# Kernel optimization log

Measured on AMD Instinct MI355X. Metric: run time of the kernel, lower is better.

The kernel has to match this reference:

```python
import jax, jax.numpy as jnp
import numpy as np

HEADS = 16
DIM_HEAD = 64


def setup_inputs() -> dict:
    key = jax.random.key(0)
    k1, k2, k3, k4, k5 = jax.random.split(key, 5)
    B, S, E = 4, 2048, 1024
    inner = HEADS * DIM_HEAD  # 1024
    return {
        "hidden_states": jax.random.normal(k1, (B, S, E), dtype=jnp.float32),
        "w_q": jax.random.normal(k2, (E, inner), dtype=jnp.float32) * (E ** -0.5),
        "w_k": jax.random.normal(k3, (E, inner), dtype=jnp.float32) * (E ** -0.5),
        "w_v": jax.random.normal(k4, (E, inner), dtype=jnp.float32) * (E ** -0.5),
        "w_o": jax.random.normal(k5, (inner, E), dtype=jnp.float32) * (inner ** -0.5),
    }


def reference(hidden_states, w_q, w_k, w_v, w_o):
    # Self-attention path: context = hidden_states (context arg is None).
    B, S, _ = hidden_states.shape
    dtype = hidden_states.dtype
    scale = DIM_HEAD ** -0.5

    q = (hidden_states @ w_q).reshape(B, S, HEADS, DIM_HEAD)
    k = (hidden_states @ w_k).reshape(B, S, HEADS, DIM_HEAD)
    v = (hidden_states @ w_v).reshape(B, S, HEADS, DIM_HEAD)

    # fp32 softmax as in the original module
    q32 = q.astype(jnp.float32)
    k32 = k.astype(jnp.float32)
    scores = jnp.einsum('btnh,bfnh->bnft', k32, q32) * scale  # [B, H, S_q, S_kv]
    probs = jax.nn.softmax(scores, axis=-1).astype(dtype)

    out = jnp.einsum('bnft,btnh->bfnh', probs, v)  # [B, S, H, D]
    out = out.reshape(B, S, HEADS * DIM_HEAD)
    return out @ w_o  # [B, S, query_dim]
```

## Files before the change

kernel.cpp:

```cpp
#include <hip/hip_runtime.h>
#include <stdint.h>

typedef __attribute__((ext_vector_type(8))) unsigned short ushort8;
typedef __attribute__((ext_vector_type(8))) __bf16 bf16x8;
typedef __attribute__((ext_vector_type(4))) float f32x4;
typedef __attribute__((ext_vector_type(4))) uint32_t u32x4;

#define TBK 32

__device__ __forceinline__ unsigned short f2bf(float f) {
  union { float f; uint32_t u; } x; x.f = f;
  uint32_t u = x.u;
  uint32_t r = (u + 0x7fffu + ((u >> 16) & 1u)) >> 16;
  return (unsigned short)r;
}

__device__ __forceinline__ uint32_t pack_bf2(float lo, float hi) {
  return (uint32_t)f2bf(lo) | ((uint32_t)f2bf(hi) << 16);
}

__device__ __forceinline__ uint32_t rhu2(float lo, float hi) {
  union { float f; uint32_t u; } a, b; a.f = lo; b.f = hi;
  return __builtin_amdgcn_perm(b.u + 0x8000u, a.u + 0x8000u, 0x07060302u);
}

__device__ __forceinline__ void store_c(unsigned short* p, float v) { *p = f2bf(v); }
__device__ __forceinline__ void store_c(float* p, float v) { *p = v; }

__device__ __forceinline__ void gll16(const unsigned short* g, unsigned short* l) {
  __builtin_amdgcn_global_load_lds((const __attribute__((address_space(1))) void*)g,
                                   (__attribute__((address_space(3))) void*)l,
                                   16, 0, 0);
}

__global__ __launch_bounds__(256) void cvt_f32_bf16(
    const float* __restrict__ x, unsigned short* __restrict__ y, int n4) {
  int i = blockIdx.x * 256 + threadIdx.x;
  if (i >= n4) return;
  float4 v = *(const float4*)(x + (size_t)i * 4);
  uint2 p; p.x = pack_bf2(v.x, v.y); p.y = pack_bf2(v.z, v.w);
  *(uint2*)(y + (size_t)i * 4) = p;
}

__global__ void transpose_w(const float* __restrict__ W,
                            unsigned short* __restrict__ WT) {
  __shared__ unsigned short tile[32][33];
  int c0 = blockIdx.x * 32, r0 = blockIdx.y * 32;
  int x = threadIdx.x, y = threadIdx.y;
#pragma unroll
  for (int i = 0; i < 32; i += 8)
    tile[y + i][x] = f2bf(W[(size_t)(r0 + y + i) * 1024 + c0 + x]);
  __syncthreads();
#pragma unroll
  for (int i = 0; i < 32; i += 8)
    WT[(size_t)(c0 + y + i) * 1024 + r0 + x] = tile[x][y + i];
}

template <typename OutT>
__global__ __launch_bounds__(256) void gemm_bt(
    const unsigned short* A,
    const unsigned short* BT0, const unsigned short* BT1, const unsigned short* BT2,
    OutT* C0, OutT* C1, OutT* C2,
    int M, int N, int K, float sc0) {
  const unsigned short* BT = (blockIdx.z == 0) ? BT0 : (blockIdx.z == 1) ? BT1 : BT2;
  OutT* C = (blockIdx.z == 0) ? C0 : (blockIdx.z == 1) ? C1 : C2;
  const float sc = (blockIdx.z == 0) ? sc0 : 1.0f;

  __shared__ __attribute__((aligned(16))) unsigned short As[128 * TBK];
  __shared__ __attribute__((aligned(16))) unsigned short Bs[128 * TBK];

  const int tid = threadIdx.x;
  const int wave = tid >> 6, lane = tid & 63;
  const int fr = lane & 15, fq = lane >> 4;
  const int bm = blockIdx.x * 128, bn = blockIdx.y * 128;
  const int wm = (wave >> 1) * 64, wn = (wave & 1) * 64;

  f32x4 acc[4][4] = {};

  const int sr = lane >> 2;
  const int sk = (lane & 3) * 8;
  const unsigned short* Ag = A + (size_t)(bm + wave * 32 + sr) * K + sk;
  const unsigned short* Bg = BT + (size_t)(bn + wave * 32 + sr) * K + sk;
  unsigned short* As0 = &As[(wave * 32) * TBK];
  unsigned short* Bs0 = &Bs[(wave * 32) * TBK];

  for (int k0 = 0; k0 < K; k0 += TBK) {
    gll16(Ag + k0, As0);
    gll16(Ag + k0 + 16 * K, As0 + 16 * TBK);
    gll16(Bg + k0, Bs0);
    gll16(Bg + k0 + 16 * K, Bs0 + 16 * TBK);
    asm volatile("s_waitcnt vmcnt(0)" ::: "memory");
    __syncthreads();

    bf16x8 af[4], bfr[4];
#pragma unroll
    for (int mt = 0; mt < 4; mt++)
      af[mt] = *(const bf16x8*)&As[(wm + mt * 16 + fr) * TBK + fq * 8];
#pragma unroll
    for (int nt = 0; nt < 4; nt++)
      bfr[nt] = *(const bf16x8*)&Bs[(wn + nt * 16 + fr) * TBK + fq * 8];
#pragma unroll
    for (int mt = 0; mt < 4; mt++)
#pragma unroll
      for (int nt = 0; nt < 4; nt++)
        acc[mt][nt] = __builtin_amdgcn_mfma_f32_16x16x32_bf16(af[mt], bfr[nt], acc[mt][nt], 0, 0, 0);
    __syncthreads();
  }

#pragma unroll
  for (int mt = 0; mt < 4; mt++)
#pragma unroll
    for (int nt = 0; nt < 4; nt++)
#pragma unroll
      for (int r = 0; r < 4; r++) {
        int row = bm + wm + mt * 16 + fq * 4 + r;
        int col = bn + wn + nt * 16 + fr;
        store_c(&C[(size_t)row * N + col], acc[mt][nt][r] * sc);
      }
}

__global__ __launch_bounds__(256, 4) void attn_kernel(
    const unsigned short* q, const unsigned short* k,
    const unsigned short* v, unsigned short* o) {
  const int S = 2048, E = 1024;
  __shared__ __attribute__((aligned(16))) unsigned short Ksb[2 * 64 * 64];
  __shared__ __attribute__((aligned(16))) unsigned short Vtb[2 * 64 * 64];

  const int tid = threadIdx.x;
  const int wave = tid >> 6, lane = tid & 63;
  const int fr = lane & 15, fq = lane >> 4;
  const int q0 = blockIdx.x * 128;
  const int bh = blockIdx.y;
  const int b = bh >> 4, h = bh & 15;
  const size_t base = ((size_t)b * S) * E + (size_t)h * 64;

  bf16x8 aq[2][2];
#pragma unroll
  for (int qg = 0; qg < 2; qg++)
#pragma unroll
    for (int ks = 0; ks < 2; ks++)
      aq[qg][ks] = *(const bf16x8*)&q[base +
          (size_t)(q0 + qg * 64 + wave * 16 + fr) * E + ks * 32 + fq * 8];

  ushort8 ones_u;
#pragma unroll
  for (int j = 0; j < 8; j++) ones_u[j] = 0x3F80;
  bf16x8 onesf = *(bf16x8*)&ones_u;

  f32x4 ot[2][4] = {};
  f32x4 osum[2] = {};

  const int srow = lane >> 3;
  const int scol = (((lane & 7) ^ srow) << 3);
  const unsigned short* Kg = k + base + (size_t)(wave * 16 + srow) * E + scol;
  unsigned short* KsW0 = &Ksb[wave * 1024];

  const int rp = (tid & 31) * 2;
  const int dcv = (tid >> 5) * 8;
  const int u_ = rp & 31;
  const int slot = 32 * (rp >> 5) + 8 * ((u_ & 15) >> 2) + 4 * (u_ >> 4) + (u_ & 3);
  const unsigned short* Vg = v + base + (size_t)rp * E + dcv;

  const int rx = (fr & 7) << 3;

  {
    gll16(Kg, KsW0);
    gll16(Kg + 8 * (size_t)E, KsW0 + 512);
    u32x4 a = *(const u32x4*)(Vg);
    u32x4 bb = *(const u32x4*)(Vg + E);
#pragma unroll
    for (int w = 0; w < 4; w++) {
      uint32_t lo = __builtin_amdgcn_perm(bb[w], a[w], 0x05040100u);
      uint32_t hi = __builtin_amdgcn_perm(bb[w], a[w], 0x07060302u);
      int d = dcv + 2 * w;
      *(uint32_t*)&Vtb[d * 64 + (slot ^ ((2 * w) << 3))] = lo;
      *(uint32_t*)&Vtb[(d + 1) * 64 + (slot ^ ((2 * w + 1) << 3))] = hi;
    }
    asm volatile("s_waitcnt vmcnt(0)" ::: "memory");
  }
  __syncthreads();

  int cur = 0;
  for (int t = 0; t < 32; t++) {
    const int nxt = cur ^ 4096;
    const bool pf = (t < 31);
    u32x4 va, vb;
    if (pf) {
      const size_t toff = (size_t)((t + 1) * 64) * E;
      va = *(const u32x4*)(Vg + toff);
      vb = *(const u32x4*)(Vg + toff + E);
      gll16(Kg + toff, &Ksb[nxt + wave * 1024]);
      gll16(Kg + toff + 8 * (size_t)E, &Ksb[nxt + wave * 1024 + 512]);
    }

    f32x4 st[2][4] = {};
#pragma unroll
    for (int ks = 0; ks < 2; ks++) {
#pragma unroll
      for (int tt = 0; tt < 4; tt++) {
        bf16x8 ak = *(const bf16x8*)&Ksb[cur + (tt * 16 + fr) * 64 +
                                         ((ks * 32 + fq * 8) ^ rx)];
        st[0][tt] = __builtin_amdgcn_mfma_f32_16x16x32_bf16(ak, aq[0][ks], st[0][tt], 0, 0, 0);
        st[1][tt] = __builtin_amdgcn_mfma_f32_16x16x32_bf16(ak, aq[1][ks], st[1][tt], 0, 0, 0);
      }
    }

    uint32_t pk[2][4][2];
#pragma unroll
    for (int qg = 0; qg < 2; qg++)
#pragma unroll
      for (int tt = 0; tt < 4; tt++) {
        float e0 = __builtin_amdgcn_exp2f(st[qg][tt][0]);
        float e1 = __builtin_amdgcn_exp2f(st[qg][tt][1]);
        float e2 = __builtin_amdgcn_exp2f(st[qg][tt][2]);
        float e3 = __builtin_amdgcn_exp2f(st[qg][tt][3]);
        pk[qg][tt][0] = rhu2(e0, e1);
        pk[qg][tt][1] = rhu2(e2, e3);
      }

    if (pf) {
#pragma unroll
      for (int w = 0; w < 4; w++) {
        uint32_t lo = __builtin_amdgcn_perm(vb[w], va[w], 0x05040100u);
        uint32_t hi = __builtin_amdgcn_perm(vb[w], va[w], 0x07060302u);
        int d = dcv + 2 * w;
        *(uint32_t*)&Vtb[nxt + d * 64 + (slot ^ ((2 * w) << 3))] = lo;
        *(uint32_t*)&Vtb[nxt + (d + 1) * 64 + (slot ^ ((2 * w + 1) << 3))] = hi;
      }
    }

#pragma unroll
    for (int c = 0; c < 2; c++) {
      bf16x8 bp[2];
#pragma unroll
      for (int qg = 0; qg < 2; qg++) {
        u32x4 bpr;
        bpr[0] = pk[qg][2 * c][0];
        bpr[1] = pk[qg][2 * c][1];
        bpr[2] = pk[qg][2 * c + 1][0];
        bpr[3] = pk[qg][2 * c + 1][1];
        bp[qg] = *(bf16x8*)&bpr;
      }
#pragma unroll
      for (int dt = 0; dt < 4; dt++) {
        bf16x8 av = *(const bf16x8*)&Vtb[cur + (dt * 16 + fr) * 64 +
                                         ((c * 32 + fq * 8) ^ rx)];
        ot[0][dt] = __builtin_amdgcn_mfma_f32_16x16x32_bf16(av, bp[0], ot[0][dt], 0, 0, 0);
        ot[1][dt] = __builtin_amdgcn_mfma_f32_16x16x32_bf16(av, bp[1], ot[1][dt], 0, 0, 0);
      }
      osum[0] = __builtin_amdgcn_mfma_f32_16x16x32_bf16(onesf, bp[0], osum[0], 0, 0, 0);
      osum[1] = __builtin_amdgcn_mfma_f32_16x16x32_bf16(onesf, bp[1], osum[1], 0, 0, 0);
    }

    if (pf) asm volatile("s_waitcnt vmcnt(0)" ::: "memory");
    __syncthreads();
    cur = nxt;
  }

#pragma unroll
  for (int qg = 0; qg < 2; qg++) {
    float inv = 1.0f / osum[qg][0];
    size_t rowbase = base + (size_t)(q0 + qg * 64 + wave * 16 + fr) * E;
#pragma unroll
    for (int dt = 0; dt < 4; dt++) {
      uint32_t w0 = rhu2(ot[qg][dt][0] * inv, ot[qg][dt][1] * inv);
      uint32_t w1 = rhu2(ot[qg][dt][2] * inv, ot[qg][dt][3] * inv);
      *(uint32_t*)&o[rowbase + dt * 16 + fq * 4] = w0;
      *(uint32_t*)&o[rowbase + dt * 16 + fq * 4 + 2] = w1;
    }
  }
}

extern "C" void kernel_launch(void* const* d_in, const int* in_sizes, int n_in,
                              void* d_out, int out_size, void* d_ws, size_t ws_size,
                              hipStream_t stream) {
  const float* hs = (const float*)d_in[0];
  const float* wq = (const float*)d_in[1];
  const float* wk = (const float*)d_in[2];
  const float* wv = (const float*)d_in[3];
  const float* wo = (const float*)d_in[4];
  unsigned short* ws = (unsigned short*)d_ws;

  unsigned short* wqT = ws;
  unsigned short* wkT = ws + 1048576;
  unsigned short* wvT = ws + 2097152;
  unsigned short* woT = wqT;
  unsigned short* qb  = ws + 3145728;
  unsigned short* kb  = qb + 8388608;
  unsigned short* vb  = kb + 8388608;
  unsigned short* ob  = qb;
  unsigned short* hsb = (unsigned short*)d_out;
  float* out = (float*)d_out;

  const int M = 8192, N = 1024, K = 1024;
  const float KSC = 0.125f * 1.44269504088896341f;

  cvt_f32_bf16<<<dim3(M * K / 4 / 256), 256, 0, stream>>>(hs, hsb, M * K / 4);

  dim3 tb(32, 8);
  transpose_w<<<dim3(32, 32), tb, 0, stream>>>(wq, wqT);
  transpose_w<<<dim3(32, 32), tb, 0, stream>>>(wk, wkT);
  transpose_w<<<dim3(32, 32), tb, 0, stream>>>(wv, wvT);

  gemm_bt<unsigned short><<<dim3(M / 128, N / 128, 3), 256, 0, stream>>>(
      hsb, wqT, wkT, wvT, qb, kb, vb, M, N, K, KSC);

  transpose_w<<<dim3(32, 32), tb, 0, stream>>>(wo, woT);

  attn_kernel<<<dim3(2048 / 128, 64), 256, 0, stream>>>(qb, kb, vb, ob);

  gemm_bt<float><<<dim3(M / 128, N / 128, 1), 256, 0, stream>>>(
      ob, woT, woT, woT, out, out, out, M, N, K, 1.0f);
}
```

Before: 296.8 us.

## Single-buffer V tile in attention loop and raise MFMA wave priority

```diff
diff --git a/kernel.cpp b/kernel.cpp
--- a/kernel.cpp
+++ b/kernel.cpp
@@ -124,7 +124,7 @@
     const unsigned short* v, unsigned short* o) {
   const int S = 2048, E = 1024;
   __shared__ __attribute__((aligned(16))) unsigned short Ksb[2 * 64 * 64];
-  __shared__ __attribute__((aligned(16))) unsigned short Vtb[2 * 64 * 64];
+  __shared__ __attribute__((aligned(16))) unsigned short Vtb[64 * 64];
 
   const int tid = threadIdx.x;
   const int wave = tid >> 6, lane = tid & 63;
@@ -153,7 +153,6 @@
   const int srow = lane >> 3;
   const int scol = (((lane & 7) ^ srow) << 3);
   const unsigned short* Kg = k + base + (size_t)(wave * 16 + srow) * E + scol;
-  unsigned short* KsW0 = &Ksb[wave * 1024];
 
   const int rp = (tid & 31) * 2;
   const int dcv = (tid >> 5) * 8;
@@ -163,37 +162,38 @@
 
   const int rx = (fr & 7) << 3;
 
-  {
-    gll16(Kg, KsW0);
-    gll16(Kg + 8 * (size_t)E, KsW0 + 512);
-    u32x4 a = *(const u32x4*)(Vg);
-    u32x4 bb = *(const u32x4*)(Vg + E);
+  gll16(Kg, &Ksb[wave * 1024]);
+  gll16(Kg + 8 * (size_t)E, &Ksb[wave * 1024 + 512]);
+
+  int cur = 0;
+  for (int t = 0; t < 32; t++) {
+    const int nxt = cur ^ 4096;
+
+    const size_t toff = (size_t)t * 64 * E;
+    u32x4 va = *(const u32x4*)(Vg + toff);
+    u32x4 vb = *(const u32x4*)(Vg + toff + E);
+
+    __syncthreads();
+
 #pragma unroll
     for (int w = 0; w < 4; w++) {
-      uint32_t lo = __builtin_amdgcn_perm(bb[w], a[w], 0x05040100u);
-      uint32_t hi = __builtin_amdgcn_perm(bb[w], a[w], 0x07060302u);
+      uint32_t lo = __builtin_amdgcn_perm(vb[w], va[w], 0x05040100u);
+      uint32_t hi = __builtin_amdgcn_perm(vb[w], va[w], 0x07060302u);
       int d = dcv + 2 * w;
       *(uint32_t*)&Vtb[d * 64 + (slot ^ ((2 * w) << 3))] = lo;
       *(uint32_t*)&Vtb[(d + 1) * 64 + (slot ^ ((2 * w + 1) << 3))] = hi;
     }
-    asm volatile("s_waitcnt vmcnt(0)" ::: "memory");
-  }
-  __syncthreads();
-
-  int cur = 0;
-  for (int t = 0; t < 32; t++) {
-    const int nxt = cur ^ 4096;
-    const bool pf = (t < 31);
-    u32x4 va, vb;
-    if (pf) {
-      const size_t toff = (size_t)((t + 1) * 64) * E;
-      va = *(const u32x4*)(Vg + toff);
-      vb = *(const u32x4*)(Vg + toff + E);
-      gll16(Kg + toff, &Ksb[nxt + wave * 1024]);
-      gll16(Kg + toff + 8 * (size_t)E, &Ksb[nxt + wave * 1024 + 512]);
+
+    __syncthreads();
+
+    if (t < 31) {
+      const size_t poff = (size_t)(t + 1) * 64 * E;
+      gll16(Kg + poff, &Ksb[nxt + wave * 1024]);
+      gll16(Kg + poff + 8 * (size_t)E, &Ksb[nxt + wave * 1024 + 512]);
     }
 
     f32x4 st[2][4] = {};
+    __builtin_amdgcn_s_setprio(1);
 #pragma unroll
     for (int ks = 0; ks < 2; ks++) {
 #pragma unroll
@@ -204,6 +204,7 @@
         st[1][tt] = __builtin_amdgcn_mfma_f32_16x16x32_bf16(ak, aq[1][ks], st[1][tt], 0, 0, 0);
       }
     }
+    __builtin_amdgcn_s_setprio(0);
 
     uint32_t pk[2][4][2];
 #pragma unroll
@@ -218,17 +219,7 @@
         pk[qg][tt][1] = rhu2(e2, e3);
       }
 
-    if (pf) {
-#pragma unroll
-      for (int w = 0; w < 4; w++) {
-        uint32_t lo = __builtin_amdgcn_perm(vb[w], va[w], 0x05040100u);
-        uint32_t hi = __builtin_amdgcn_perm(vb[w], va[w], 0x07060302u);
-        int d = dcv + 2 * w;
-        *(uint32_t*)&Vtb[nxt + d * 64 + (slot ^ ((2 * w) << 3))] = lo;
-        *(uint32_t*)&Vtb[nxt + (d + 1) * 64 + (slot ^ ((2 * w + 1) << 3))] = hi;
-      }
-    }
-
+    __builtin_amdgcn_s_setprio(1);
 #pragma unroll
     for (int c = 0; c < 2; c++) {
       bf16x8 bp[2];
@@ -243,7 +234,7 @@
       }
 #pragma unroll
       for (int dt = 0; dt < 4; dt++) {
-        bf16x8 av = *(const bf16x8*)&Vtb[cur + (dt * 16 + fr) * 64 +
+        bf16x8 av = *(const bf16x8*)&Vtb[(dt * 16 + fr) * 64 +
                                          ((c * 32 + fq * 8) ^ rx)];
         ot[0][dt] = __builtin_amdgcn_mfma_f32_16x16x32_bf16(av, bp[0], ot[0][dt], 0, 0, 0);
         ot[1][dt] = __builtin_amdgcn_mfma_f32_16x16x32_bf16(av, bp[1], ot[1][dt], 0, 0, 0);
@@ -251,9 +242,8 @@
       osum[0] = __builtin_amdgcn_mfma_f32_16x16x32_bf16(onesf, bp[0], osum[0], 0, 0, 0);
       osum[1] = __builtin_amdgcn_mfma_f32_16x16x32_bf16(onesf, bp[1], osum[1], 0, 0, 0);
     }
-
-    if (pf) asm volatile("s_waitcnt vmcnt(0)" ::: "memory");
-    __syncthreads();
+    __builtin_amdgcn_s_setprio(0);
+
     cur = nxt;
   }
 
```

Result: faster. 279.1 us (-6.0%).
